# Kernel optimization log

Measured on AMD Instinct MI355X. Metric: run time of the kernel, lower is better.

## Reference

```python
import jax, jax.numpy as jnp
import numpy as np

MAX_ACF_LAG = 6
TOP_K_FFT = 3
CLIP_VALUE = 5.0
EPS = 1e-8


def setup_inputs() -> dict:
    key = jax.random.key(0)
    x = jax.random.normal(key, (128, 4096, 32), dtype=jnp.float32)
    return {"x": x}


def _per_var_features(x):
    # x: [B, T, V] -> [B, V, 10 + MAX_ACF_LAG]
    B, T, V = x.shape
    mean = jnp.mean(x, axis=1)                      # [B, V]
    xc = x - mean[:, None, :]                       # centered, [B, T, V]
    var = jnp.mean(xc * xc, axis=1)                 # [B, V]
    std = jnp.sqrt(var + EPS)
    z = xc / std[:, None, :]
    skew = jnp.mean(z ** 3, axis=1)
    kurt = jnp.mean(z ** 4, axis=1)
    mn = jnp.min(x, axis=1)
    mx = jnp.max(x, axis=1)
    # linear trend slope via least squares on t = 0..T-1
    t = jnp.arange(T, dtype=x.dtype)
    tc = t - jnp.mean(t)
    slope = jnp.einsum('btv,t->bv', xc, tc) / jnp.sum(tc * tc)
    # top-k FFT magnitudes (exclude DC), normalized by T
    mag = jnp.abs(jnp.fft.rfft(x, axis=1))[:, 1:, :] / T   # [B, F, V]
    topk, _ = jax.lax.top_k(jnp.transpose(mag, (0, 2, 1)), TOP_K_FFT)  # [B, V, k]
    # autocorrelation at lags 1..MAX_ACF_LAG
    denom = jnp.sum(xc * xc, axis=1) + EPS          # [B, V]
    acfs = [jnp.sum(xc[:, :-lag, :] * xc[:, lag:, :], axis=1) / denom
            for lag in range(1, MAX_ACF_LAG + 1)]
    acf = jnp.stack(acfs, axis=-1)                  # [B, V, L]
    base = jnp.stack([mean, std, skew, kurt, mn, mx, slope], axis=-1)  # [B, V, 7]
    return jnp.concatenate([base, topk, acf], axis=-1)  # [B, V, 16]


def reference(x):
    feats = _per_var_features(x)                    # [B, V, 16]
    f_mean = jnp.mean(feats, axis=1)                # [B, 16]
    f_std = jnp.std(feats, axis=1)                  # [B, 16]
    out = jnp.concatenate([f_mean, f_std], axis=-1) # [B, 32]
    return jnp.clip(out, -CLIP_VALUE, CLIP_VALUE)
```

## Files before the change

kernel.cpp:

```cpp
#include <hip/hip_runtime.h>
#include <math.h>

#define T_LEN 4096
#define M_LEN 2048
#define V_DIM 32
#define B_DIM 128
#define NTHREADS 256
#define NWAVES 4
#define NSERIES 4096
#define FS NSERIES

__device__ __forceinline__ int SW(int i) {
    return i ^ (((i >> 4) & 7) << 1) ^ (((i >> 7) & 15) << 1);
}

__device__ __forceinline__ int fpos(int k) {
    return ((k & 3) << 9) | (((k >> 2) & 3) << 7) | (((k >> 4) & 3) << 5)
         | (((k >> 6) & 3) << 3) | (((k >> 8) & 3) << 1) | ((k >> 10) & 1);
}

__device__ __forceinline__ void ins3(float& a0, float& a1, float& a2, float m) {
    if (m > a0) { a2 = a1; a1 = a0; a0 = m; }
    else if (m > a1) { a2 = a1; a1 = m; }
    else if (m > a2) { a2 = m; }
}

#define SCR_A_PART 0
#define SCR_A_FIN  12
#define SCR_B_PART 16
#define SCR_B_FIN  176
#define SCR_C_PART 186
#define SCR_SIZE   200

__device__ __forceinline__ void bfly4(float2* Z, int base, int q,
                                      float sn, float cs, float c2, float s2,
                                      float c3, float s3) {
    const int p0 = SW(base), p1 = SW(base + q);
    const int p2i = SW(base + 2 * q), p3 = SW(base + 3 * q);
    float2 a = Z[p0], bb = Z[p1], c = Z[p2i], d = Z[p3];
    float t0r = a.x + c.x,  t0i = a.y + c.y;
    float t1r = a.x - c.x,  t1i = a.y - c.y;
    float t2r = bb.x + d.x, t2i = bb.y + d.y;
    float t3r = bb.x - d.x, t3i = bb.y - d.y;
    float y1r = t1r + t3i, y1i = t1i - t3r;
    float y2r = t0r - t2r, y2i = t0i - t2i;
    float y3r = t1r - t3i, y3i = t1i + t3r;
    Z[p0]  = make_float2(t0r + t2r, t0i + t2i);
    Z[p1]  = make_float2(y1r * cs - y1i * sn, y1r * sn + y1i * cs);
    Z[p2i] = make_float2(y2r * c2 - y2i * s2, y2r * s2 + y2i * c2);
    Z[p3]  = make_float2(y3r * c3 - y3i * s3, y3r * s3 + y3i * c3);
}

template <int ST>
__device__ __forceinline__ void fft_stage(float2* Z, int tid) {
    constexpr int lq = 9 - 2 * ST;
    constexpr int q  = 1 << lq;
    const float scale = -3.06796158e-3f * (float)(1 << (2 * ST));
    if constexpr (ST == 0) {
        #pragma unroll
        for (int i = 0; i < 2; i++) {
            const int w = tid + (i << 8);
            const int g = w >> lq;
            const int j = w & (q - 1);
            float sn, cs;
            __sincosf(scale * (float)j, &sn, &cs);
            const float c2 = cs * cs - sn * sn, s2 = 2.f * cs * sn;
            const float c3 = c2 * cs - s2 * sn, s3 = c2 * sn + s2 * cs;
            bfly4(Z, (g << (lq + 2)) + j, q, sn, cs, c2, s2, c3, s3);
        }
    } else {
        const int j = tid & (q - 1);
        float sn, cs;
        __sincosf(scale * (float)j, &sn, &cs);
        const float c2 = cs * cs - sn * sn, s2 = 2.f * cs * sn;
        const float c3 = c2 * cs - s2 * sn, s3 = c2 * sn + s2 * cs;
        #pragma unroll
        for (int i = 0; i < 2; i++) {
            const int g = (tid + (i << 8)) >> lq;
            bfly4(Z, (g << (lq + 2)) + j, q, sn, cs, c2, s2, c3, s3);
        }
    }
}

__device__ __forceinline__ void fft_stage4_r2(float2* Z, int tid) {
    const int base = tid * 8;
    float4 P0 = *reinterpret_cast<const float4*>(&Z[SW(base)]);
    float4 P2 = *reinterpret_cast<const float4*>(&Z[SW(base + 2)]);
    float4 P4 = *reinterpret_cast<const float4*>(&Z[SW(base + 4)]);
    float4 P6 = *reinterpret_cast<const float4*>(&Z[SW(base + 6)]);
    float t0r = P0.x + P4.x, t0i = P0.y + P4.y;
    float t1r = P0.x - P4.x, t1i = P0.y - P4.y;
    float t2r = P2.x + P6.x, t2i = P2.y + P6.y;
    float t3r = P2.x - P6.x, t3i = P2.y - P6.y;
    float o0r = t0r + t2r, o0i = t0i + t2i;
    float o2r = t1r + t3i, o2i = t1i - t3r;
    float o4r = t0r - t2r, o4i = t0i - t2i;
    float o6r = t1r - t3i, o6i = t1i + t3r;
    const float C = 0.70710678118654752f;
    float u0r = P0.z + P4.z, u0i = P0.w + P4.w;
    float u1r = P0.z - P4.z, u1i = P0.w - P4.w;
    float u2r = P2.z + P6.z, u2i = P2.w + P6.w;
    float u3r = P2.z - P6.z, u3i = P2.w - P6.w;
    float o1r = u0r + u2r, o1i = u0i + u2i;
    float y1r = u1r + u3i, y1i = u1i - u3r;
    float o3r = C * (y1r + y1i), o3i = C * (y1i - y1r);
    float y2r = u0r - u2r, y2i = u0i - u2i;
    float o5r = y2i, o5i = -y2r;
    float y3r = u1r - u3i, y3i = u1i + u3r;
    float o7r = C * (y3i - y3r), o7i = -C * (y3r + y3i);
    float4 R0 = make_float4(o0r + o1r, o0i + o1i, o0r - o1r, o0i - o1i);
    float4 R2 = make_float4(o2r + o3r, o2i + o3i, o2r - o3r, o2i - o3i);
    float4 R4 = make_float4(o4r + o5r, o4i + o5i, o4r - o5r, o4i - o5i);
    float4 R6 = make_float4(o6r + o7r, o6i + o7i, o6r - o7r, o6i - o7i);
    *reinterpret_cast<float4*>(&Z[SW(base)])     = R0;
    *reinterpret_cast<float4*>(&Z[SW(base + 2)]) = R2;
    *reinterpret_cast<float4*>(&Z[SW(base + 4)]) = R4;
    *reinterpret_cast<float4*>(&Z[SW(base + 6)]) = R6;
}

__global__ __launch_bounds__(NTHREADS, 8)
void ts_feat_kernel(const float* __restrict__ x, float* __restrict__ feats) {
    __shared__ __align__(16) float data[T_LEN];
    __shared__ float scr[SCR_SIZE];
    float2* const Z = reinterpret_cast<float2*>(&data[0]);

    const int tid = threadIdx.x;
    const int bid = blockIdx.x;
    const int xcd = bid & 7;
    const int idx = bid >> 3;
    const int b   = xcd + ((idx >> 5) << 3);
    const int v   = idx & 31;
    const int sid = b * V_DIM + v;

    const float* __restrict__ px = x + (size_t)b * T_LEN * V_DIM + v;

    float xr[16];
    #pragma unroll
    for (int u = 0; u < 16; u++) {
        xr[u] = px[(size_t)(16 * tid + u) * V_DIM];
    }
    float s = 0.f, mn = 3.4e38f, mx = -3.4e38f;
    #pragma unroll
    for (int u = 0; u < 16; u++) {
        s += xr[u]; mn = fminf(mn, xr[u]); mx = fmaxf(mx, xr[u]);
    }
    const int fb2 = tid * 8;
    #pragma unroll
    for (int u4 = 0; u4 < 4; u4++) {
        float4 q = make_float4(xr[4 * u4], xr[4 * u4 + 1], xr[4 * u4 + 2], xr[4 * u4 + 3]);
        *reinterpret_cast<float4*>(&Z[SW(fb2 + 2 * u4)]) = q;
    }
    #pragma unroll
    for (int o = 32; o > 0; o >>= 1) {
        s += __shfl_down(s, o);
        mn = fminf(mn, __shfl_down(mn, o));
        mx = fmaxf(mx, __shfl_down(mx, o));
    }
    const int lane = tid & 63, wv = tid >> 6;
    if (lane == 0) {
        scr[SCR_A_PART + wv * 3 + 0] = s;
        scr[SCR_A_PART + wv * 3 + 1] = mn;
        scr[SCR_A_PART + wv * 3 + 2] = mx;
    }
    __syncthreads();

    float2 tv = make_float2(0.f, 0.f);
    float4 tq = make_float4(0.f, 0.f, 0.f, 0.f);
    if (tid > 0) {
        tv = Z[SW(fb2 - 3)];
        tq = *reinterpret_cast<const float4*>(&Z[SW(fb2 - 2)]);
    }
    if (tid < 3) {
        float r = scr[SCR_A_PART + tid];
        #pragma unroll
        for (int w = 1; w < NWAVES; w++) {
            float vv = scr[SCR_A_PART + w * 3 + tid];
            r = (tid == 0) ? (r + vv) : ((tid == 1) ? fminf(r, vv) : fmaxf(r, vv));
        }
        scr[SCR_A_FIN + tid] = r;
    }
    __syncthreads();
    const float m = scr[SCR_A_FIN + 0] * (1.f / T_LEN);

    {
        float q2 = 0.f, q3 = 0.f, q4 = 0.f, qt = 0.f;
        float l1 = 0.f, l2 = 0.f, l3 = 0.f, l4 = 0.f, l5 = 0.f, l6 = 0.f;
        float p1v, p2v, p3v, p4v, p5v, p6v;
        if (tid > 0) {
            p6v = tv.x - m; p5v = tv.y - m;
            p4v = tq.x - m; p3v = tq.y - m; p2v = tq.z - m; p1v = tq.w - m;
        } else {
            p1v = p2v = p3v = p4v = p5v = p6v = 0.f;
        }
        const float tf0 = (float)(tid * 16) - 2047.5f;
        #pragma unroll
        for (int u = 0; u < 16; u++) {
            float c = xr[u] - m;
            float cc = c * c;
            q2 += cc; q3 += cc * c; q4 += cc * cc;
            qt += c * (tf0 + (float)u);
            l1 += p1v * c; l2 += p2v * c; l3 += p3v * c;
            l4 += p4v * c; l5 += p5v * c; l6 += p6v * c;
            p6v = p5v; p5v = p4v; p4v = p3v; p3v = p2v; p2v = p1v; p1v = c;
        }
        #pragma unroll
        for (int o = 32; o >= 4; o >>= 1) {
            q2 += __shfl_down(q2, o); q3 += __shfl_down(q3, o);
            q4 += __shfl_down(q4, o); qt += __shfl_down(qt, o);
            l1 += __shfl_down(l1, o); l2 += __shfl_down(l2, o);
            l3 += __shfl_down(l3, o); l4 += __shfl_down(l4, o);
            l5 += __shfl_down(l5, o); l6 += __shfl_down(l6, o);
        }
        if (lane < 4) {
            float* part = &scr[SCR_B_PART + wv * 40 + lane * 10];
            part[0] = q2; part[1] = q3; part[2] = q4; part[3] = qt;
            part[4] = l1; part[5] = l2; part[6] = l3;
            part[7] = l4; part[8] = l5; part[9] = l6;
        }
    }
    __syncthreads();

    if (tid < 10) {
        float acc = 0.f;
        #pragma unroll
        for (int e = 0; e < 16; e++) acc += scr[SCR_B_PART + e * 10 + tid];
        scr[SCR_B_FIN + tid] = acc;
    }
    fft_stage<0>(Z, tid);
    __syncthreads();

    if (tid == 0) {
        const float* A = &scr[SCR_B_FIN];
        float c2 = A[0], c3 = A[1], c4 = A[2], ct = A[3];
        float var = c2 * (1.f / T_LEN);
        float sd  = sqrtf(var + 1e-8f);
        float i3  = 1.f / (sd * sd * sd);
        float dn  = c2 + 1e-8f;
        float* fp = feats + sid;
        fp[0 * FS] = m; fp[1 * FS] = sd;
        fp[2 * FS] = c3 * (1.f / T_LEN) * i3;
        fp[3 * FS] = c4 * (1.f / T_LEN) * i3 / sd;
        fp[4 * FS] = scr[SCR_A_FIN + 1]; fp[5 * FS] = scr[SCR_A_FIN + 2];
        fp[6 * FS] = ct / 5726622720.f;
        fp[10 * FS] = A[4] / dn; fp[11 * FS] = A[5] / dn; fp[12 * FS] = A[6] / dn;
        fp[13 * FS] = A[7] / dn; fp[14 * FS] = A[8] / dn; fp[15 * FS] = A[9] / dn;
    }
    fft_stage<1>(Z, tid);
    __syncthreads();
    fft_stage<2>(Z, tid);
    __syncthreads();
    fft_stage<3>(Z, tid);
    __syncthreads();
    fft_stage4_r2(Z, tid);
    __syncthreads();

    const float inv_T = 1.f / (float)T_LEN;
    float a0 = -1.f, a1 = -1.f, a2 = -1.f;
    #pragma unroll
    for (int i = 0; i < 4; i++) {
        int k  = 1 + tid + (i << 8);
        int pa = fpos(k);
        int pb = fpos(M_LEN - k);
        float ang = (float)k * (-3.14159265358979f / (float)M_LEN);
        float sn, cs; __sincosf(ang, &sn, &cs);
        float2 Za = Z[SW(pa)], Zb = Z[SW(pb)];
        float Er = 0.5f * (Za.x + Zb.x), Ei = 0.5f * (Za.y - Zb.y);
        float Or = 0.5f * (Za.y + Zb.y), Oi = 0.5f * (Zb.x - Za.x);
        float u = cs * Or - sn * Oi, vv = cs * Oi + sn * Or;
        float Xr = Er + u, Xi = Ei + vv;
        ins3(a0, a1, a2, Xr * Xr + Xi * Xi);
        if (k != 1024) {
            float Yr = Er - u, Yi = vv - Ei;
            ins3(a0, a1, a2, Yr * Yr + Yi * Yi);
        }
    }
    if (tid == 0) {
        float2 Z0 = Z[SW(0)];
        float d = Z0.x - Z0.y;
        ins3(a0, a1, a2, d * d);
    }
    #pragma unroll
    for (int o = 32; o > 0; o >>= 1) {
        float u0 = __shfl_down(a0, o), u1 = __shfl_down(a1, o), u2 = __shfl_down(a2, o);
        ins3(a0, a1, a2, u0); ins3(a0, a1, a2, u1); ins3(a0, a1, a2, u2);
    }
    if (lane == 0) {
        scr[SCR_C_PART + wv * 3 + 0] = a0;
        scr[SCR_C_PART + wv * 3 + 1] = a1;
        scr[SCR_C_PART + wv * 3 + 2] = a2;
    }
    __syncthreads();
    if (tid == 0) {
        float t0 = scr[SCR_C_PART], t1 = scr[SCR_C_PART + 1], t2 = scr[SCR_C_PART + 2];
        #pragma unroll
        for (int w = 1; w < NWAVES; w++) {
            ins3(t0, t1, t2, scr[SCR_C_PART + w * 3 + 0]);
            ins3(t0, t1, t2, scr[SCR_C_PART + w * 3 + 1]);
            ins3(t0, t1, t2, scr[SCR_C_PART + w * 3 + 2]);
        }
        float* fp = feats + sid;
        fp[7 * FS] = sqrtf(t0) * inv_T;
        fp[8 * FS] = sqrtf(t1) * inv_T;
        fp[9 * FS] = sqrtf(t2) * inv_T;
    }
}

__global__ __launch_bounds__(256)
void ts_reduce_kernel(const float* __restrict__ feats, float* __restrict__ out) {
    const int tid = threadIdx.x;
    const int lane = tid & 63;
    const int wid = blockIdx.x * 4 + (tid >> 6);
    const int pairidx = wid * 2 + (lane >> 5);
    const int b = pairidx >> 4, f = pairidx & 15;
    const int v = lane & 31;
    float val = feats[f * FS + b * V_DIM + v];
    float s = val;
    #pragma unroll
    for (int o = 16; o > 0; o >>= 1) s += __shfl_xor(s, o);
    float m = s * (1.f / V_DIM);
    float d = val - m;
    float q = d * d;
    #pragma unroll
    for (int o = 16; o > 0; o >>= 1) q += __shfl_xor(q, o);
    float sd = sqrtf(q * (1.f / V_DIM));
    if (v == 0) {
        out[b * 32 + f]      = fminf(fmaxf(m,  -5.f), 5.f);
        out[b * 32 + 16 + f] = fminf(fmaxf(sd, -5.f), 5.f);
    }
}

extern "C" void kernel_launch(void* const* d_in, const int* in_sizes, int n_in,
                              void* d_out, int out_size, void* d_ws, size_t ws_size,
                              hipStream_t stream) {
    const float* x = (const float*)d_in[0];
    float* out = (float*)d_out;
    float* feats = (float*)d_ws;

    hipLaunchKernelGGL(ts_feat_kernel, dim3(NSERIES), dim3(NTHREADS), 0, stream,
                       x, feats);
    hipLaunchKernelGGL(ts_reduce_kernel, dim3(256), dim3(256), 0, stream,
                       feats, out);
}
```

Baseline: 125.8 us.

## Process each series with a single wavefront, removing block barriers

```diff
diff --git a/kernel.cpp b/kernel.cpp
--- a/kernel.cpp
+++ b/kernel.cpp
@@ -5,8 +5,7 @@
 #define M_LEN 2048
 #define V_DIM 32
 #define B_DIM 128
-#define NTHREADS 256
-#define NWAVES 4
+#define NTHREADS 64
 #define NSERIES 4096
 #define FS NSERIES
 
@@ -24,13 +23,6 @@
     else if (m > a1) { a2 = a1; a1 = m; }
     else if (m > a2) { a2 = m; }
 }
-
-#define SCR_A_PART 0
-#define SCR_A_FIN  12
-#define SCR_B_PART 16
-#define SCR_B_FIN  176
-#define SCR_C_PART 186
-#define SCR_SIZE   200
 
 __device__ __forceinline__ void bfly4(float2* Z, int base, int q,
                                       float sn, float cs, float c2, float s2,
@@ -52,14 +44,25 @@
 }
 
 template <int ST>
-__device__ __forceinline__ void fft_stage(float2* Z, int tid) {
+__device__ __forceinline__ void fft_stage_w(float2* Z, int L) {
     constexpr int lq = 9 - 2 * ST;
     constexpr int q  = 1 << lq;
     const float scale = -3.06796158e-3f * (float)(1 << (2 * ST));
-    if constexpr (ST == 0) {
-        #pragma unroll
-        for (int i = 0; i < 2; i++) {
-            const int w = tid + (i << 8);
+    if constexpr (ST >= 2) {
+        const int j = L & (q - 1);
+        float sn, cs;
+        __sincosf(scale * (float)j, &sn, &cs);
+        const float c2 = cs * cs - sn * sn, s2 = 2.f * cs * sn;
+        const float c3 = c2 * cs - s2 * sn, s3 = c2 * sn + s2 * cs;
+        #pragma unroll
+        for (int i = 0; i < 8; i++) {
+            const int g = (L + (i << 6)) >> lq;
+            bfly4(Z, (g << (lq + 2)) + j, q, sn, cs, c2, s2, c3, s3);
+        }
+    } else {
+        #pragma unroll
+        for (int i = 0; i < 8; i++) {
+            const int w = L + (i << 6);
             const int g = w >> lq;
             const int j = w & (q - 1);
             float sn, cs;
@@ -68,22 +71,10 @@
             const float c3 = c2 * cs - s2 * sn, s3 = c2 * sn + s2 * cs;
             bfly4(Z, (g << (lq + 2)) + j, q, sn, cs, c2, s2, c3, s3);
         }
-    } else {
-        const int j = tid & (q - 1);
-        float sn, cs;
-        __sincosf(scale * (float)j, &sn, &cs);
-        const float c2 = cs * cs - sn * sn, s2 = 2.f * cs * sn;
-        const float c3 = c2 * cs - s2 * sn, s3 = c2 * sn + s2 * cs;
-        #pragma unroll
-        for (int i = 0; i < 2; i++) {
-            const int g = (tid + (i << 8)) >> lq;
-            bfly4(Z, (g << (lq + 2)) + j, q, sn, cs, c2, s2, c3, s3);
-        }
-    }
-}
-
-__device__ __forceinline__ void fft_stage4_r2(float2* Z, int tid) {
-    const int base = tid * 8;
+    }
+}
+
+__device__ __forceinline__ void fft_blk8(float2* Z, int base) {
     float4 P0 = *reinterpret_cast<const float4*>(&Z[SW(base)]);
     float4 P2 = *reinterpret_cast<const float4*>(&Z[SW(base + 2)]);
     float4 P4 = *reinterpret_cast<const float4*>(&Z[SW(base + 4)]);
@@ -118,13 +109,12 @@
     *reinterpret_cast<float4*>(&Z[SW(base + 6)]) = R6;
 }
 
-__global__ __launch_bounds__(NTHREADS, 8)
+__global__ __launch_bounds__(NTHREADS, 10)
 void ts_feat_kernel(const float* __restrict__ x, float* __restrict__ feats) {
     __shared__ __align__(16) float data[T_LEN];
-    __shared__ float scr[SCR_SIZE];
     float2* const Z = reinterpret_cast<float2*>(&data[0]);
 
-    const int tid = threadIdx.x;
+    const int L = threadIdx.x;
     const int bid = blockIdx.x;
     const int xcd = bid & 7;
     const int idx = bid >> 3;
@@ -134,21 +124,20 @@
 
     const float* __restrict__ px = x + (size_t)b * T_LEN * V_DIM + v;
 
-    float xr[16];
-    #pragma unroll
-    for (int u = 0; u < 16; u++) {
-        xr[u] = px[(size_t)(16 * tid + u) * V_DIM];
-    }
     float s = 0.f, mn = 3.4e38f, mx = -3.4e38f;
     #pragma unroll
-    for (int u = 0; u < 16; u++) {
-        s += xr[u]; mn = fminf(mn, xr[u]); mx = fmaxf(mx, xr[u]);
-    }
-    const int fb2 = tid * 8;
-    #pragma unroll
-    for (int u4 = 0; u4 < 4; u4++) {
-        float4 q = make_float4(xr[4 * u4], xr[4 * u4 + 1], xr[4 * u4 + 2], xr[4 * u4 + 3]);
-        *reinterpret_cast<float4*>(&Z[SW(fb2 + 2 * u4)]) = q;
+    for (int c = 0; c < 8; c++) {
+        float x8[8];
+        #pragma unroll
+        for (int u = 0; u < 8; u++)
+            x8[u] = px[(size_t)(64 * L + 8 * c + u) * V_DIM];
+        #pragma unroll
+        for (int u = 0; u < 8; u++) {
+            s += x8[u]; mn = fminf(mn, x8[u]); mx = fmaxf(mx, x8[u]);
+        }
+        const int f2b = 32 * L + 4 * c;
+        *reinterpret_cast<float4*>(&Z[SW(f2b)])     = make_float4(x8[0], x8[1], x8[2], x8[3]);
+        *reinterpret_cast<float4*>(&Z[SW(f2b + 2)]) = make_float4(x8[4], x8[5], x8[6], x8[7]);
     }
     #pragma unroll
     for (int o = 32; o > 0; o >>= 1) {
@@ -156,109 +145,79 @@
         mn = fminf(mn, __shfl_down(mn, o));
         mx = fmaxf(mx, __shfl_down(mx, o));
     }
-    const int lane = tid & 63, wv = tid >> 6;
-    if (lane == 0) {
-        scr[SCR_A_PART + wv * 3 + 0] = s;
-        scr[SCR_A_PART + wv * 3 + 1] = mn;
-        scr[SCR_A_PART + wv * 3 + 2] = mx;
-    }
-    __syncthreads();
-
-    float2 tv = make_float2(0.f, 0.f);
-    float4 tq = make_float4(0.f, 0.f, 0.f, 0.f);
-    if (tid > 0) {
-        tv = Z[SW(fb2 - 3)];
-        tq = *reinterpret_cast<const float4*>(&Z[SW(fb2 - 2)]);
-    }
-    if (tid < 3) {
-        float r = scr[SCR_A_PART + tid];
-        #pragma unroll
-        for (int w = 1; w < NWAVES; w++) {
-            float vv = scr[SCR_A_PART + w * 3 + tid];
-            r = (tid == 0) ? (r + vv) : ((tid == 1) ? fminf(r, vv) : fmaxf(r, vv));
-        }
-        scr[SCR_A_FIN + tid] = r;
-    }
-    __syncthreads();
-    const float m = scr[SCR_A_FIN + 0] * (1.f / T_LEN);
+    const float m = __shfl(s, 0) * (1.f / T_LEN);
+    __builtin_amdgcn_sched_barrier(0);
 
     {
         float q2 = 0.f, q3 = 0.f, q4 = 0.f, qt = 0.f;
         float l1 = 0.f, l2 = 0.f, l3 = 0.f, l4 = 0.f, l5 = 0.f, l6 = 0.f;
         float p1v, p2v, p3v, p4v, p5v, p6v;
-        if (tid > 0) {
+        if (L > 0) {
+            float2 tv = Z[SW(32 * L - 3)];
+            float4 tq = *reinterpret_cast<const float4*>(&Z[SW(32 * L - 2)]);
             p6v = tv.x - m; p5v = tv.y - m;
             p4v = tq.x - m; p3v = tq.y - m; p2v = tq.z - m; p1v = tq.w - m;
         } else {
             p1v = p2v = p3v = p4v = p5v = p6v = 0.f;
         }
-        const float tf0 = (float)(tid * 16) - 2047.5f;
-        #pragma unroll
-        for (int u = 0; u < 16; u++) {
-            float c = xr[u] - m;
-            float cc = c * c;
-            q2 += cc; q3 += cc * c; q4 += cc * cc;
-            qt += c * (tf0 + (float)u);
-            l1 += p1v * c; l2 += p2v * c; l3 += p3v * c;
-            l4 += p4v * c; l5 += p5v * c; l6 += p6v * c;
-            p6v = p5v; p5v = p4v; p4v = p3v; p3v = p2v; p2v = p1v; p1v = c;
-        }
-        #pragma unroll
-        for (int o = 32; o >= 4; o >>= 1) {
+        const float tf0 = (float)(L * 64) - 2047.5f;
+        #pragma unroll
+        for (int c = 0; c < 8; c++) {
+            float4 qa = *reinterpret_cast<const float4*>(&Z[SW(32 * L + 4 * c)]);
+            float4 qb = *reinterpret_cast<const float4*>(&Z[SW(32 * L + 4 * c + 2)]);
+            float x8[8] = {qa.x, qa.y, qa.z, qa.w, qb.x, qb.y, qb.z, qb.w};
+            #pragma unroll
+            for (int u = 0; u < 8; u++) {
+                float cv = x8[u] - m;
+                float cc = cv * cv;
+                q2 += cc; q3 += cc * cv; q4 += cc * cc;
+                qt += cv * (tf0 + (float)(8 * c + u));
+                l1 += p1v * cv; l2 += p2v * cv; l3 += p3v * cv;
+                l4 += p4v * cv; l5 += p5v * cv; l6 += p6v * cv;
+                p6v = p5v; p5v = p4v; p4v = p3v; p3v = p2v; p2v = p1v; p1v = cv;
+            }
+        }
+        #pragma unroll
+        for (int o = 32; o > 0; o >>= 1) {
             q2 += __shfl_down(q2, o); q3 += __shfl_down(q3, o);
             q4 += __shfl_down(q4, o); qt += __shfl_down(qt, o);
             l1 += __shfl_down(l1, o); l2 += __shfl_down(l2, o);
             l3 += __shfl_down(l3, o); l4 += __shfl_down(l4, o);
             l5 += __shfl_down(l5, o); l6 += __shfl_down(l6, o);
         }
-        if (lane < 4) {
-            float* part = &scr[SCR_B_PART + wv * 40 + lane * 10];
-            part[0] = q2; part[1] = q3; part[2] = q4; part[3] = qt;
-            part[4] = l1; part[5] = l2; part[6] = l3;
-            part[7] = l4; part[8] = l5; part[9] = l6;
-        }
-    }
-    __syncthreads();
-
-    if (tid < 10) {
-        float acc = 0.f;
-        #pragma unroll
-        for (int e = 0; e < 16; e++) acc += scr[SCR_B_PART + e * 10 + tid];
-        scr[SCR_B_FIN + tid] = acc;
-    }
-    fft_stage<0>(Z, tid);
-    __syncthreads();
-
-    if (tid == 0) {
-        const float* A = &scr[SCR_B_FIN];
-        float c2 = A[0], c3 = A[1], c4 = A[2], ct = A[3];
-        float var = c2 * (1.f / T_LEN);
-        float sd  = sqrtf(var + 1e-8f);
-        float i3  = 1.f / (sd * sd * sd);
-        float dn  = c2 + 1e-8f;
-        float* fp = feats + sid;
-        fp[0 * FS] = m; fp[1 * FS] = sd;
-        fp[2 * FS] = c3 * (1.f / T_LEN) * i3;
-        fp[3 * FS] = c4 * (1.f / T_LEN) * i3 / sd;
-        fp[4 * FS] = scr[SCR_A_FIN + 1]; fp[5 * FS] = scr[SCR_A_FIN + 2];
-        fp[6 * FS] = ct / 5726622720.f;
-        fp[10 * FS] = A[4] / dn; fp[11 * FS] = A[5] / dn; fp[12 * FS] = A[6] / dn;
-        fp[13 * FS] = A[7] / dn; fp[14 * FS] = A[8] / dn; fp[15 * FS] = A[9] / dn;
-    }
-    fft_stage<1>(Z, tid);
-    __syncthreads();
-    fft_stage<2>(Z, tid);
-    __syncthreads();
-    fft_stage<3>(Z, tid);
-    __syncthreads();
-    fft_stage4_r2(Z, tid);
-    __syncthreads();
+        if (L == 0) {
+            float c2t = q2, c3t = q3, c4t = q4, ct = qt;
+            float var = c2t * (1.f / T_LEN);
+            float sd  = sqrtf(var + 1e-8f);
+            float i3  = 1.f / (sd * sd * sd);
+            float dn  = c2t + 1e-8f;
+            float* fp = feats + sid;
+            fp[0 * FS] = m; fp[1 * FS] = sd;
+            fp[2 * FS] = c3t * (1.f / T_LEN) * i3;
+            fp[3 * FS] = c4t * (1.f / T_LEN) * i3 / sd;
+            fp[4 * FS] = mn; fp[5 * FS] = mx;
+            fp[6 * FS] = ct / 5726622720.f;
+            fp[10 * FS] = l1 / dn; fp[11 * FS] = l2 / dn; fp[12 * FS] = l3 / dn;
+            fp[13 * FS] = l4 / dn; fp[14 * FS] = l5 / dn; fp[15 * FS] = l6 / dn;
+        }
+    }
+    __builtin_amdgcn_sched_barrier(0);
+
+    fft_stage_w<0>(Z, L);  __builtin_amdgcn_sched_barrier(0);
+    fft_stage_w<1>(Z, L);  __builtin_amdgcn_sched_barrier(0);
+    fft_stage_w<2>(Z, L);  __builtin_amdgcn_sched_barrier(0);
+    fft_stage_w<3>(Z, L);  __builtin_amdgcn_sched_barrier(0);
+    #pragma unroll
+    for (int i = 0; i < 4; i++) {
+        fft_blk8(Z, (L + (i << 6)) * 8);
+    }
+    __builtin_amdgcn_sched_barrier(0);
 
     const float inv_T = 1.f / (float)T_LEN;
     float a0 = -1.f, a1 = -1.f, a2 = -1.f;
     #pragma unroll
-    for (int i = 0; i < 4; i++) {
-        int k  = 1 + tid + (i << 8);
+    for (int i = 0; i < 16; i++) {
+        int k  = 1 + L + (i << 6);
         int pa = fpos(k);
         int pb = fpos(M_LEN - k);
         float ang = (float)k * (-3.14159265358979f / (float)M_LEN);
@@ -274,7 +233,7 @@
             ins3(a0, a1, a2, Yr * Yr + Yi * Yi);
         }
     }
-    if (tid == 0) {
+    if (L == 0) {
         float2 Z0 = Z[SW(0)];
         float d = Z0.x - Z0.y;
         ins3(a0, a1, a2, d * d);
@@ -284,24 +243,11 @@
         float u0 = __shfl_down(a0, o), u1 = __shfl_down(a1, o), u2 = __shfl_down(a2, o);
         ins3(a0, a1, a2, u0); ins3(a0, a1, a2, u1); ins3(a0, a1, a2, u2);
     }
-    if (lane == 0) {
-        scr[SCR_C_PART + wv * 3 + 0] = a0;
-        scr[SCR_C_PART + wv * 3 + 1] = a1;
-        scr[SCR_C_PART + wv * 3 + 2] = a2;
-    }
-    __syncthreads();
-    if (tid == 0) {
-        float t0 = scr[SCR_C_PART], t1 = scr[SCR_C_PART + 1], t2 = scr[SCR_C_PART + 2];
-        #pragma unroll
-        for (int w = 1; w < NWAVES; w++) {
-            ins3(t0, t1, t2, scr[SCR_C_PART + w * 3 + 0]);
-            ins3(t0, t1, t2, scr[SCR_C_PART + w * 3 + 1]);
-            ins3(t0, t1, t2, scr[SCR_C_PART + w * 3 + 2]);
-        }
+    if (L == 0) {
         float* fp = feats + sid;
-        fp[7 * FS] = sqrtf(t0) * inv_T;
-        fp[8 * FS] = sqrtf(t1) * inv_T;
-        fp[9 * FS] = sqrtf(t2) * inv_T;
+        fp[7 * FS] = sqrtf(a0) * inv_T;
+        fp[8 * FS] = sqrtf(a1) * inv_T;
+        fp[9 * FS] = sqrtf(a2) * inv_T;
     }
 }
 
```

Measured after the change: 128.4 us. +2.1%, slower.
